# Kernel optimization log

Measured on AMD Instinct MI355X. Metric: run time of the kernel, lower is better.

Reference implementation:

```python
import jax, jax.numpy as jnp
import numpy as np

E = 1024        # embedding_dim
DIN = 2048      # d_inner = E * expand_factor(2)
N = 16          # state_dim
DTR = 64        # dt_rank = ceil(E/16)
K_CONV = 4      # conv_dim


def tt_dense(g1, g2):
    # TT with ranks [1,16,1]: W[(m1,m2),(n1,n2)] = sum_r g1[m1,n1,r] g2[r,m2,n2]
    m1, n1, r = g1.shape
    _, m2, n2 = g2.shape
    return jnp.einsum('air,rbj->abij', g1, g2).reshape(m1 * m2, n1 * n2)


def setup_inputs() -> dict:
    key = jax.random.key(0)
    ks = jax.random.split(key, 12)
    s = 0.05  # init scale for TT cores
    return {
        'x': jax.random.normal(ks[0], (2, 1024, E), dtype=jnp.float32),
        # in_proj: 1024=[32,32] -> 4096=[64,64]
        'in_g1': jax.random.normal(ks[1], (32, 64, 16)) * s,
        'in_g2': jax.random.normal(ks[2], (16, 32, 64)) * s,
        # x_proj: 2048=[32,64] -> 96=[8,12]
        'x_g1': jax.random.normal(ks[3], (32, 8, 16)) * s,
        'x_g2': jax.random.normal(ks[4], (16, 64, 12)) * s,
        # dt_proj: 64=[8,8] -> 2048=[32,64]
        'dt_g1': jax.random.normal(ks[5], (8, 32, 16)) * s,
        'dt_g2': jax.random.normal(ks[6], (16, 8, 64)) * s,
        # out_proj: 2048=[32,64] -> 1024=[32,32]
        'out_g1': jax.random.normal(ks[7], (32, 32, 16)) * s,
        'out_g2': jax.random.normal(ks[8], (16, 64, 32)) * s,
        'conv_filter': jax.random.normal(ks[9], (K_CONV, 1, DIN)) * 0.1,
        'conv_bias': jnp.zeros((DIN,), jnp.float32),
        'A_log': jax.random.uniform(ks[10], (DIN, N), dtype=jnp.float32),
        'D': jnp.zeros((DIN,), jnp.float32),
    }


def _forward(x, in_g1, in_g2, x_g1, x_g2, dt_g1, dt_g2, out_g1, out_g2,
             conv_filter, conv_bias, A_log, D):
    B, L, _ = x.shape
    # in_proj (TT) -> split into conv path and gate
    xz = (x.reshape(-1, E) @ tt_dense(in_g1, in_g2)).reshape(B, L, 2 * DIN)
    x_conv, z = xz[..., :DIN], xz[..., DIN:]
    # depthwise conv1d, SAME padding, + bias, SiLU, gate by z
    conv = jax.lax.conv_general_dilated(
        x_conv, conv_filter, window_strides=(1,), padding='SAME',
        dimension_numbers=('NWC', 'WIO', 'NWC'), feature_group_count=DIN)
    y = jax.nn.silu(conv + conv_bias) * z            # [B, L, DIN]
    # x_proj (TT) -> dt_unscaled, B, C
    dtBC = (y.reshape(-1, DIN) @ tt_dense(x_g1, x_g2)).reshape(B, L, DTR + 2 * N)
    dt_un = dtBC[..., :DTR]
    Bm = dtBC[..., DTR:DTR + N]                      # [B, L, N]
    Cm = dtBC[..., DTR + N:]                         # [B, L, N]
    # dt_proj (TT) + softplus
    dt = jax.nn.softplus(dt_un.reshape(-1, DTR) @ tt_dense(dt_g1, dt_g2)).reshape(B, L, DIN)
    # selective scan
    A = -jnp.exp(A_log)                              # [DIN, N]

    def step(h, inp):
        dt_t, u_t, B_t, C_t = inp                    # [B,DIN],[B,DIN],[B,N],[B,N]
        dA = jnp.exp(dt_t[:, :, None] * A)           # [B, DIN, N]
        h = dA * h + dt_t[:, :, None] * B_t[:, None, :] * u_t[:, :, None]
        y_t = jnp.einsum('bdn,bn->bd', h, C_t) + D * u_t
        return h, (y_t, h)

    h0 = jnp.zeros((B, DIN, N), x.dtype)
    _, (ys, hs) = jax.lax.scan(
        step, h0,
        (dt.swapaxes(0, 1), y.swapaxes(0, 1), Bm.swapaxes(0, 1), Cm.swapaxes(0, 1)))
    ssm_out = ys.swapaxes(0, 1) + jnp.mean(hs) * 1e-8  # [B, L, DIN]
    out = (ssm_out.reshape(-1, DIN) @ tt_dense(out_g1, out_g2)).reshape(B, L, E)
    return out


def reference(x, in_g1, in_g2, x_g1, x_g2, dt_g1, dt_g2, out_g1, out_g2,
              conv_filter, conv_bias, A_log, D):
    return _forward(x, in_g1, in_g2, x_g1, x_g2, dt_g1, dt_g2, out_g1, out_g2,
                    conv_filter, conv_bias, A_log, D)
```

## Files before the change

### kernel.cpp

```cpp
#include <hip/hip_runtime.h>
#include <hip/hip_bf16.h>
#include <cstdint>
#include <cstddef>

#define EE    1024
#define DIN   2048
#define NST   16
#define DTR   64
#define BB_   2
#define LL    1024
#define BL    (BB_*LL)
#define NCHUNK 16
#define CLEN   64
#define RTT   16

typedef unsigned short u16;
typedef unsigned int   u32;

static constexpr size_t OFF_WINT  = 0;
static constexpr size_t OFF_WOUTT = 2097152;
static constexpr size_t OFF_WXT   = 3145728;
static constexpr size_t OFF_WDTT  = 3276800;
static constexpr size_t OFF_A2T   = 3342336;
static constexpr size_t OFF_XB    = 3375104;
static constexpr size_t OFF_XZB   = 4423680;
static constexpr size_t OFF_YB    = 8617984;
static constexpr size_t OFF_PART  = 10715136;
static constexpr size_t OFF_DTBC  = 14909440;
static constexpr size_t OFF_DTUNB = 15106048;
static constexpr size_t OFF_DTB   = 15171584;
static constexpr size_t OFF_YSB   = 17268736;
static constexpr size_t OFF_HC    = 19365888;
static constexpr size_t OFF_SDT   = 20414464;

__device__ __forceinline__ u16 f2bf(float f) {
    u32 u = __float_as_uint(f);
    u += 0x7fffu + ((u >> 16) & 1u);
    return (u16)(u >> 16);
}
__device__ __forceinline__ float bf2f(u16 v) {
    return __uint_as_float((u32)v << 16);
}

__device__ __forceinline__ void async_copy16(const void* g, void* l) {
    __builtin_amdgcn_global_load_lds((const __attribute__((address_space(1))) u32*)g,
                                     (__attribute__((address_space(3))) u32*)l,
                                     16, 0, 0);
}

__device__ __forceinline__ float softplusf(float v) {
    return fmaxf(v, 0.f) + log1pf(__expf(-fabsf(v)));
}

__device__ void tt_part(const float* __restrict__ g1, const float* __restrict__ g2,
                        u16* __restrict__ Wt, int m1, int n1, int m2, int n2,
                        int c, int crows, float* g1col, float* g2col)
{
    const int rowsW = m1 * m2;
    if (c >= crows) {
        for (int k = threadIdx.x; k < rowsW; k += 256)
            Wt[(size_t)c * rowsW + k] = 0;
        return;
    }
    const int i = c / n2;
    const int j = c - i * n2;

    for (int e = threadIdx.x; e < m1 * RTT; e += 256) {
        const int a = e >> 4, rr = e & 15;
        g1col[e] = g1[(size_t)(a * n1 + i) * RTT + rr];
    }
    for (int e = threadIdx.x; e < RTT * m2; e += 256) {
        const int rr = e / m2, bb = e - rr * m2;
        g2col[e] = g2[(size_t)(rr * m2 + bb) * n2 + j];
    }
    __syncthreads();

    for (int k = threadIdx.x; k < rowsW; k += 256) {
        const int a  = k / m2;
        const int bb = k - a * m2;
        const float* gp = g1col + a * RTT;
        float s = 0.f;
        #pragma unroll
        for (int rr = 0; rr < RTT; ++rr)
            s = fmaf(gp[rr], g2col[rr * m2 + bb], s);
        Wt[(size_t)c * rowsW + k] = f2bf(s);
    }
}

__global__ __launch_bounds__(256) void mega_prep(
    const float* __restrict__ in_g1, const float* __restrict__ in_g2, u16* __restrict__ W_inT,
    const float* __restrict__ out_g1, const float* __restrict__ out_g2, u16* __restrict__ W_outT,
    const float* __restrict__ x_g1, const float* __restrict__ x_g2, u16* __restrict__ W_xT,
    const float* __restrict__ dt_g1, const float* __restrict__ dt_g2, u16* __restrict__ W_dtT,
    const float* __restrict__ x, u16* __restrict__ xb,
    const float* __restrict__ A_log, float* __restrict__ A2t)
{
    __shared__ float g1col[32 * RTT];
    __shared__ float g2col[RTT * 64];
    const int blk = blockIdx.x;
    if (blk < 4096) {
        tt_part(in_g1, in_g2, W_inT, 32, 64, 32, 64, blk, 4096, g1col, g2col);
    } else if (blk < 5120) {
        tt_part(out_g1, out_g2, W_outT, 32, 32, 64, 32, blk - 4096, 1024, g1col, g2col);
    } else if (blk < 5248) {
        tt_part(x_g1, x_g2, W_xT, 32, 8, 64, 12, blk - 5120, 96, g1col, g2col);
    } else if (blk < 7296) {
        tt_part(dt_g1, dt_g2, W_dtT, 8, 32, 8, 64, blk - 5248, 2048, g1col, g2col);
    } else if (blk < 9344) {
        const int i = (blk - 7296) * 256 + threadIdx.x;
        float4 v = ((const float4*)x)[i];
        ushort4 o;
        o.x = f2bf(v.x); o.y = f2bf(v.y); o.z = f2bf(v.z); o.w = f2bf(v.w);
        ((ushort4*)xb)[i] = o;
    } else {
        const int idx = (blk - 9344) * 256 + threadIdx.x;
        const int d = idx >> 4, n = idx & 15;
        A2t[n * DIN + d] = -expf(A_log[idx]);
    }
}

typedef __attribute__((ext_vector_type(8))) short bf16x8;
typedef __attribute__((ext_vector_type(4))) float floatx4;

template<int BN, int BK, int OUT>
__global__ __launch_bounds__(256) void gemm_bf16(
    const u16* __restrict__ A, const u16* __restrict__ Bt, void* __restrict__ Cout,
    int K, int ldc, int kchunk, size_t czstride)
{
    constexpr int BM   = 128;
    constexpr int NT   = BN / 32;
    constexpr int SLOT = BK / 8;
    constexpr int CR   = 64 / SLOT;
    constexpr int NACH = BM / CR / 4;
    constexpr int NBCH = BN / CR / 4;
    constexpr int KG   = BK / 32;
    __shared__ u16 As[BM * BK];
    __shared__ u16 Bs[BN * BK];

    const int tid  = threadIdx.x;
    const int w    = tid >> 6;
    const int lane = tid & 63;
    const int wm   = w & 1, wn = w >> 1;
    const int row0 = blockIdx.y * BM;
    const int col0 = blockIdx.x * BN;
    const int kbeg = blockIdx.z * kchunk;

    const int srow = lane / SLOT;
    const int kqp  = lane % SLOT;
    const u16* ga[NACH]; u16* la[NACH];
    #pragma unroll
    for (int i = 0; i < NACH; ++i) {
        const int c  = w * NACH + i;
        const int r  = c * CR + srow;
        const int kq = kqp ^ ((r >> 1) & (SLOT - 1));
        ga[i] = A + (size_t)(row0 + r) * K + kbeg + kq * 8;
        la[i] = &As[c * CR * BK];
    }
    const u16* gb[NBCH]; u16* lb[NBCH];
    #pragma unroll
    for (int i = 0; i < NBCH; ++i) {
        const int c  = w * NBCH + i;
        const int r  = c * CR + srow;
        const int kq = kqp ^ ((r >> 1) & (SLOT - 1));
        gb[i] = Bt + (size_t)(col0 + r) * K + kbeg + kq * 8;
        lb[i] = &Bs[c * CR * BK];
    }

    const int q = lane >> 4, l15 = lane & 15;
    int a_off[4][KG], b_off[NT][KG];
    #pragma unroll
    for (int mt = 0; mt < 4; ++mt) {
        const int r = wm * 64 + mt * 16 + l15;
        const int m = (r >> 1) & (SLOT - 1);
        #pragma unroll
        for (int kk = 0; kk < KG; ++kk)
            a_off[mt][kk] = r * BK + ((kk * 4 + q) ^ m) * 8;
    }
    #pragma unroll
    for (int nt = 0; nt < NT; ++nt) {
        const int r = wn * (BN / 2) + nt * 16 + l15;
        const int m = (r >> 1) & (SLOT - 1);
        #pragma unroll
        for (int kk = 0; kk < KG; ++kk)
            b_off[nt][kk] = r * BK + ((kk * 4 + q) ^ m) * 8;
    }

    floatx4 acc[4][NT];
    #pragma unroll
    for (int mt = 0; mt < 4; ++mt)
        #pragma unroll
        for (int nt = 0; nt < NT; ++nt)
            acc[mt][nt] = (floatx4){0.f, 0.f, 0.f, 0.f};

    for (int k0 = 0; k0 < kchunk; k0 += BK) {
        #pragma unroll
        for (int i = 0; i < NACH; ++i) { async_copy16(ga[i], la[i]); ga[i] += BK; }
        #pragma unroll
        for (int i = 0; i < NBCH; ++i) { async_copy16(gb[i], lb[i]); gb[i] += BK; }
        __syncthreads();

        bf16x8 af[4][KG], bfv[NT][KG];
        #pragma unroll
        for (int mt = 0; mt < 4; ++mt)
            #pragma unroll
            for (int kk = 0; kk < KG; ++kk)
                af[mt][kk] = *(const bf16x8*)&As[a_off[mt][kk]];
        #pragma unroll
        for (int nt = 0; nt < NT; ++nt)
            #pragma unroll
            for (int kk = 0; kk < KG; ++kk)
                bfv[nt][kk] = *(const bf16x8*)&Bs[b_off[nt][kk]];

        #pragma unroll
        for (int kk = 0; kk < KG; ++kk)
            #pragma unroll
            for (int mt = 0; mt < 4; ++mt)
                #pragma unroll
                for (int nt = 0; nt < NT; ++nt)
                    acc[mt][nt] = __builtin_amdgcn_mfma_f32_16x16x32_bf16(
                        af[mt][kk], bfv[nt][kk], acc[mt][nt], 0, 0, 0);

        __syncthreads();
    }

    #pragma unroll
    for (int mt = 0; mt < 4; ++mt) {
        const int row = row0 + wm * 64 + mt * 16 + q * 4;
        #pragma unroll
        for (int nt = 0; nt < NT; ++nt) {
            const int col = col0 + wn * (BN / 2) + nt * 16 + l15;
            #pragma unroll
            for (int r = 0; r < 4; ++r) {
                const float v = acc[mt][nt][r];
                if constexpr (OUT == 0) {
                    ((float*)Cout)[(size_t)blockIdx.z * czstride + (size_t)(row + r) * ldc + col] = v;
                } else if constexpr (OUT == 1) {
                    ((u16*)Cout)[(size_t)(row + r) * ldc + col] = f2bf(v);
                } else {
                    ((u16*)Cout)[(size_t)(row + r) * ldc + col] = f2bf(softplusf(v));
                }
            }
        }
    }
}

__global__ __launch_bounds__(256) void reduce_dtbc(
    const float* __restrict__ part, float* __restrict__ dtBC, u16* __restrict__ dtun_b)
{
    int idx = blockIdx.x * 256 + threadIdx.x;
    if (idx >= BL * 96) return;
    const int row = idx / 96;
    const int col = idx - row * 96;
    float s = 0.f;
    #pragma unroll
    for (int z = 0; z < 16; ++z)
        s += part[(size_t)z * BL * 128 + (size_t)row * 128 + col];
    dtBC[idx] = s;
    if (col < 64) dtun_b[(size_t)row * 64 + col] = f2bf(s);
}

__global__ __launch_bounds__(256) void conv_gate(
    const u16* __restrict__ xzb, const float* __restrict__ filt,
    const float* __restrict__ bias, u16* __restrict__ yb)
{
    int idx = blockIdx.x * blockDim.x + threadIdx.x;
    if (idx >= BL * DIN / 4) return;
    const int d  = (idx % (DIN / 4)) * 4;
    const int bt = idx / (DIN / 4);
    const int b  = bt >> 10;
    const int t  = bt & 1023;

    float4 acc = *(const float4*)(bias + d);
    #pragma unroll
    for (int k = 0; k < 4; ++k) {
        const int tt = t + k - 1;
        if ((unsigned)tt < (unsigned)LL) {
            const ushort4 xc = *(const ushort4*)(xzb + (size_t)(b * LL + tt) * (2 * DIN) + d);
            const float4 f  = *(const float4*)(filt + (size_t)k * DIN + d);
            acc.x = fmaf(bf2f(xc.x), f.x, acc.x);
            acc.y = fmaf(bf2f(xc.y), f.y, acc.y);
            acc.z = fmaf(bf2f(xc.z), f.z, acc.z);
            acc.w = fmaf(bf2f(xc.w), f.w, acc.w);
        }
    }
    const ushort4 z = *(const ushort4*)(xzb + (size_t)bt * (2 * DIN) + DIN + d);
    ushort4 o;
    o.x = f2bf(acc.x / (1.f + __expf(-acc.x)) * bf2f(z.x));
    o.y = f2bf(acc.y / (1.f + __expf(-acc.y)) * bf2f(z.y));
    o.z = f2bf(acc.z / (1.f + __expf(-acc.z)) * bf2f(z.z));
    o.w = f2bf(acc.w / (1.f + __expf(-acc.w)) * bf2f(z.w));
    *(ushort4*)(yb + (size_t)bt * DIN + d) = o;
}

__global__ __launch_bounds__(256) void scan_phase_a(
    const u16* __restrict__ dt, const u16* __restrict__ u,
    const float* __restrict__ dtBC, const float* __restrict__ A2t,
    float* __restrict__ hend, float* __restrict__ sdtbuf)
{
    const int d = blockIdx.x * 256 + threadIdx.x;
    const int c = blockIdx.y;
    const int b = blockIdx.z;

    __shared__ float Bs[CLEN][NST];
    for (int e = threadIdx.x; e < CLEN * NST; e += 256) {
        const int tl = e >> 4, n = e & 15;
        Bs[tl][n] = dtBC[(size_t)(b * LL + c * CLEN + tl) * 96 + 64 + n];
    }
    __syncthreads();

    float A2r[NST];
    #pragma unroll
    for (int n = 0; n < NST; ++n) A2r[n] = A2t[n * DIN + d];

    float h[NST] = {};
    float sdt = 0.f;
    const size_t tbase = (size_t)(b * LL + c * CLEN) * DIN + d;
    for (int tl = 0; tl < CLEN; ++tl) {
        const float dtv = bf2f(dt[tbase + (size_t)tl * DIN]);
        const float uv  = bf2f(u [tbase + (size_t)tl * DIN]);
        sdt += dtv;
        const float cu = dtv * uv;
        #pragma unroll
        for (int n = 0; n < NST; ++n) {
            const float a = __expf(A2r[n] * dtv);
            h[n] = fmaf(a, h[n], cu * Bs[tl][n]);
        }
    }
    const int cb = b * NCHUNK + c;
    #pragma unroll
    for (int n = 0; n < NST; ++n)
        hend[((size_t)cb * NST + n) * DIN + d] = h[n];
    sdtbuf[(size_t)cb * DIN + d] = sdt;
}

__global__ __launch_bounds__(256) void scan_phase_b(
    const float* __restrict__ A2t, const float* __restrict__ sdtbuf,
    float* __restrict__ hcarry)
{
    const int idx = blockIdx.x * 256 + threadIdx.x;
    if (idx >= BB_ * NST * DIN) return;
    const int d = idx & (DIN - 1);
    const int n = (idx >> 11) & 15;
    const int b = idx >> 15;
    const float A2 = A2t[n * DIN + d];
    float h = 0.f;
    for (int c = 0; c < NCHUNK; ++c) {
        const int cb = b * NCHUNK + c;
        const size_t off = ((size_t)cb * NST + n) * DIN + d;
        const float he = hcarry[off];
        const float pa = __expf(A2 * sdtbuf[(size_t)cb * DIN + d]);
        hcarry[off] = h;
        h = fmaf(pa, h, he);
    }
}

__global__ __launch_bounds__(256) void scan_phase_c(
    const u16* __restrict__ dt, const u16* __restrict__ u,
    const float* __restrict__ dtBC, const float* __restrict__ A2t,
    const float* __restrict__ hinit, const float* __restrict__ Dp,
    u16* __restrict__ ysb)
{
    const int d = blockIdx.x * 256 + threadIdx.x;
    const int c = blockIdx.y;
    const int b = blockIdx.z;

    __shared__ float Bs[CLEN][NST];
    __shared__ float Cs[CLEN][NST];
    for (int e = threadIdx.x; e < CLEN * NST; e += 256) {
        const int tl = e >> 4, n = e & 15;
        const size_t base = (size_t)(b * LL + c * CLEN + tl) * 96;
        Bs[tl][n] = dtBC[base + 64 + n];
        Cs[tl][n] = dtBC[base + 80 + n];
    }
    __syncthreads();

    float A2r[NST], h[NST];
    const int cb = b * NCHUNK + c;
    #pragma unroll
    for (int n = 0; n < NST; ++n) {
        A2r[n] = A2t[n * DIN + d];
        h[n]   = hinit[((size_t)cb * NST + n) * DIN + d];
    }
    const float Dv = Dp[d];

    const size_t tbase = (size_t)(b * LL + c * CLEN) * DIN + d;
    for (int tl = 0; tl < CLEN; ++tl) {
        const float dtv = bf2f(dt[tbase + (size_t)tl * DIN]);
        const float uv  = bf2f(u [tbase + (size_t)tl * DIN]);
        const float cu = dtv * uv;
        float yacc = 0.f;
        #pragma unroll
        for (int n = 0; n < NST; ++n) {
            const float a = __expf(A2r[n] * dtv);
            h[n] = fmaf(a, h[n], cu * Bs[tl][n]);
            yacc = fmaf(h[n], Cs[tl][n], yacc);
        }
        ysb[tbase + (size_t)tl * DIN] = f2bf(fmaf(Dv, uv, yacc));
    }
}

extern "C" void kernel_launch(void* const* d_in, const int* in_sizes, int n_in,
                              void* d_out, int out_size, void* d_ws, size_t ws_size,
                              hipStream_t stream)
{
    const float* x       = (const float*)d_in[0];
    const float* in_g1   = (const float*)d_in[1];
    const float* in_g2   = (const float*)d_in[2];
    const float* x_g1    = (const float*)d_in[3];
    const float* x_g2    = (const float*)d_in[4];
    const float* dt_g1   = (const float*)d_in[5];
    const float* dt_g2   = (const float*)d_in[6];
    const float* out_g1  = (const float*)d_in[7];
    const float* out_g2  = (const float*)d_in[8];
    const float* filt    = (const float*)d_in[9];
    const float* bias    = (const float*)d_in[10];
    const float* A_log   = (const float*)d_in[11];
    const float* Dp      = (const float*)d_in[12];

    float* ws     = (float*)d_ws;
    u16*   W_inT  = (u16*)(ws + OFF_WINT);
    u16*   W_outT = (u16*)(ws + OFF_WOUTT);
    u16*   W_xT   = (u16*)(ws + OFF_WXT);
    u16*   W_dtT  = (u16*)(ws + OFF_WDTT);
    float* A2t    = ws + OFF_A2T;
    u16*   xb     = (u16*)(ws + OFF_XB);
    u16*   xzb    = (u16*)(ws + OFF_XZB);
    u16*   yb     = (u16*)(ws + OFF_YB);
    float* part   = ws + OFF_PART;
    float* dtBC   = ws + OFF_DTBC;
    u16*   dtun_b = (u16*)(ws + OFF_DTUNB);
    u16*   dtb    = (u16*)(ws + OFF_DTB);
    u16*   ysb    = (u16*)(ws + OFF_YSB);
    float* hc     = ws + OFF_HC;
    float* sdt    = ws + OFF_SDT;

    mega_prep<<<9472, 256, 0, stream>>>(
        in_g1, in_g2, W_inT, out_g1, out_g2, W_outT,
        x_g1, x_g2, W_xT, dt_g1, dt_g2, W_dtT,
        x, xb, A_log, A2t);

    gemm_bf16<128, 32, 1><<<dim3(32, 16, 1), 256, 0, stream>>>(
        xb, W_inT, xzb, EE, 4096, EE, 0);

    conv_gate<<<(BL * DIN / 4 + 255) / 256, 256, 0, stream>>>(xzb, filt, bias, yb);

    gemm_bf16<128, 64, 0><<<dim3(1, 16, 16), 256, 0, stream>>>(
        yb, W_xT, part, DIN, 128, 128, (size_t)BL * 128);
    reduce_dtbc<<<(BL * 96 + 255) / 256, 256, 0, stream>>>(part, dtBC, dtun_b);

    gemm_bf16<128, 64, 2><<<dim3(16, 16, 1), 256, 0, stream>>>(
        dtun_b, W_dtT, dtb, 64, DIN, 64, 0);

    scan_phase_a<<<dim3(DIN / 256, NCHUNK, BB_), 256, 0, stream>>>(dtb, yb, dtBC, A2t, hc, sdt);
    scan_phase_b<<<(BB_ * NST * DIN) / 256, 256, 0, stream>>>(A2t, sdt, hc);
    scan_phase_c<<<dim3(DIN / 256, NCHUNK, BB_), 256, 0, stream>>>(dtb, yb, dtBC, A2t, hc, Dp, ysb);

    gemm_bf16<64, 64, 0><<<dim3(16, 16, 1), 256, 0, stream>>>(
        ysb, W_outT, (float*)d_out, DIN, EE, DIN, 0);
}
```

Baseline: 262.5 us.

## Split-K out_proj, widen conv vectors, retune scan chunks and in_proj tile

The out_proj GEMM now runs as a two-way split-K into a partial buffer, followed by a new reduce kernel. This doubles the block count for that GEMM at the cost of extra memory traffic. The scan moves from 16 chunks of 64 to 32 chunks of 32 for more parallelism in phases A and C, at the price of a longer sequential phase B. conv_gate now processes 8 bf16 elements per thread instead of 4, and the in_proj GEMM tile template changes from 32 to 64.

```diff
diff --git a/kernel.cpp b/kernel.cpp
--- a/kernel.cpp
+++ b/kernel.cpp
@@ -10,8 +10,8 @@
 #define BB_   2
 #define LL    1024
 #define BL    (BB_*LL)
-#define NCHUNK 16
-#define CLEN   64
+#define NCHUNK 32
+#define CLEN   32
 #define RTT   16
 
 typedef unsigned short u16;
@@ -31,7 +31,7 @@
 static constexpr size_t OFF_DTB   = 15171584;
 static constexpr size_t OFF_YSB   = 17268736;
 static constexpr size_t OFF_HC    = 19365888;
-static constexpr size_t OFF_SDT   = 20414464;
+static constexpr size_t OFF_SDT   = 21463040;
 
 __device__ __forceinline__ u16 f2bf(float f) {
     u32 u = __float_as_uint(f);
@@ -259,37 +259,49 @@
     if (col < 64) dtun_b[(size_t)row * 64 + col] = f2bf(s);
 }
 
+__global__ __launch_bounds__(256) void reduce_out(
+    const float* __restrict__ part, float* __restrict__ out)
+{
+    const int idx = blockIdx.x * 256 + threadIdx.x;
+    const float4 a = ((const float4*)part)[idx];
+    const float4 b = ((const float4*)part)[idx + BL * EE / 4];
+    float4 o;
+    o.x = a.x + b.x; o.y = a.y + b.y; o.z = a.z + b.z; o.w = a.w + b.w;
+    ((float4*)out)[idx] = o;
+}
+
+typedef __attribute__((ext_vector_type(8))) unsigned short ushortx8;
+
 __global__ __launch_bounds__(256) void conv_gate(
     const u16* __restrict__ xzb, const float* __restrict__ filt,
     const float* __restrict__ bias, u16* __restrict__ yb)
 {
     int idx = blockIdx.x * blockDim.x + threadIdx.x;
-    if (idx >= BL * DIN / 4) return;
-    const int d  = (idx % (DIN / 4)) * 4;
-    const int bt = idx / (DIN / 4);
+    if (idx >= BL * DIN / 8) return;
+    const int d  = (idx % (DIN / 8)) * 8;
+    const int bt = idx / (DIN / 8);
     const int b  = bt >> 10;
     const int t  = bt & 1023;
 
-    float4 acc = *(const float4*)(bias + d);
+    float acc[8];
+    #pragma unroll
+    for (int j = 0; j < 8; ++j) acc[j] = bias[d + j];
     #pragma unroll
     for (int k = 0; k < 4; ++k) {
         const int tt = t + k - 1;
         if ((unsigned)tt < (unsigned)LL) {
-            const ushort4 xc = *(const ushort4*)(xzb + (size_t)(b * LL + tt) * (2 * DIN) + d);
-            const float4 f  = *(const float4*)(filt + (size_t)k * DIN + d);
-            acc.x = fmaf(bf2f(xc.x), f.x, acc.x);
-            acc.y = fmaf(bf2f(xc.y), f.y, acc.y);
-            acc.z = fmaf(bf2f(xc.z), f.z, acc.z);
-            acc.w = fmaf(bf2f(xc.w), f.w, acc.w);
+            const ushortx8 xc = *(const ushortx8*)(xzb + (size_t)(b * LL + tt) * (2 * DIN) + d);
+            #pragma unroll
+            for (int j = 0; j < 8; ++j)
+                acc[j] = fmaf(bf2f(xc[j]), filt[(size_t)k * DIN + d + j], acc[j]);
         }
     }
-    const ushort4 z = *(const ushort4*)(xzb + (size_t)bt * (2 * DIN) + DIN + d);
-    ushort4 o;
-    o.x = f2bf(acc.x / (1.f + __expf(-acc.x)) * bf2f(z.x));
-    o.y = f2bf(acc.y / (1.f + __expf(-acc.y)) * bf2f(z.y));
-    o.z = f2bf(acc.z / (1.f + __expf(-acc.z)) * bf2f(z.z));
-    o.w = f2bf(acc.w / (1.f + __expf(-acc.w)) * bf2f(z.w));
-    *(ushort4*)(yb + (size_t)bt * DIN + d) = o;
+    const ushortx8 z = *(const ushortx8*)(xzb + (size_t)bt * (2 * DIN) + DIN + d);
+    ushortx8 o;
+    #pragma unroll
+    for (int j = 0; j < 8; ++j)
+        o[j] = f2bf(acc[j] / (1.f + __expf(-acc[j])) * bf2f(z[j]));
+    *(ushortx8*)(yb + (size_t)bt * DIN + d) = o;
 }
 
 __global__ __launch_bounds__(256) void scan_phase_a(
@@ -439,10 +451,10 @@
         x_g1, x_g2, W_xT, dt_g1, dt_g2, W_dtT,
         x, xb, A_log, A2t);
 
-    gemm_bf16<128, 32, 1><<<dim3(32, 16, 1), 256, 0, stream>>>(
+    gemm_bf16<128, 64, 1><<<dim3(32, 16, 1), 256, 0, stream>>>(
         xb, W_inT, xzb, EE, 4096, EE, 0);
 
-    conv_gate<<<(BL * DIN / 4 + 255) / 256, 256, 0, stream>>>(xzb, filt, bias, yb);
+    conv_gate<<<(BL * DIN / 8 + 255) / 256, 256, 0, stream>>>(xzb, filt, bias, yb);
 
     gemm_bf16<128, 64, 0><<<dim3(1, 16, 16), 256, 0, stream>>>(
         yb, W_xT, part, DIN, 128, 128, (size_t)BL * 128);
@@ -455,6 +467,7 @@
     scan_phase_b<<<(BB_ * NST * DIN) / 256, 256, 0, stream>>>(A2t, sdt, hc);
     scan_phase_c<<<dim3(DIN / 256, NCHUNK, BB_), 256, 0, stream>>>(dtb, yb, dtBC, A2t, hc, Dp, ysb);
 
-    gemm_bf16<64, 64, 0><<<dim3(16, 16, 1), 256, 0, stream>>>(
-        ysb, W_outT, (float*)d_out, DIN, EE, DIN, 0);
-}
+    gemm_bf16<64, 64, 0><<<dim3(16, 16, 2), 256, 0, stream>>>(
+        ysb, W_outT, part, DIN, EE, EE, (size_t)BL * EE);
+    reduce_out<<<(BL * EE / 4) / 256, 256, 0, stream>>>(part, (float*)d_out);
+}
```

Measured after the change: 228.3 us. -13.0%, faster.
